# Optimization experiments

Measured on AMD Instinct MI355X. Metric: run time of the kernel, lower is better.

Reference implementation:

```python
import jax, jax.numpy as jnp
import numpy as np

MAX_WORDS = 50257
INPUT_SIZE = 1024
BATCH, SEQ = 8, 2048


def setup_inputs() -> dict:
    key = jax.random.key(0)
    kx, kw, kb = jax.random.split(key, 3)
    x = jax.random.randint(kx, (BATCH, SEQ), 0, MAX_WORDS, dtype=jnp.int64 if jax.config.jax_enable_x64 else jnp.int32)
    # nn.Linear(max_words, input_size): weight [input_size, max_words], bias [input_size]
    W = jax.random.normal(kw, (INPUT_SIZE, MAX_WORDS), dtype=jnp.float32) * 0.02
    b = jax.random.normal(kb, (INPUT_SIZE,), dtype=jnp.float32) * 0.02
    return {"x": x, "W": W, "b": b}


def reference(x, W, b):
    # one_hot(x, V).float() @ W.T + b  ==  gather rows of W.T at x, plus bias.
    # W.T has shape [max_words, input_size]; result [B, S, input_size].
    return jnp.take(W.T, x, axis=0) + b
```

## Files before the change

### kernel.cpp

```cpp
#include <hip/hip_runtime.h>


#define VOCAB 50257
#define DIM   1024
#define NBUCK ((VOCAB + 15) >> 4)
#define NXCD  8
#define TPB   64
#define JSL   128
#define NJS   (DIM / JSL)
#define TSTR  65


__global__ void hist_kernel(const int* __restrict__ x, int n, int* __restrict__ counts) {
    int i = blockIdx.x * blockDim.x + threadIdx.x;
    if (i < n) atomicAdd(&counts[x[i] >> 4], 1);
}

__global__ __launch_bounds__(256) void scan_kernel(const int* __restrict__ counts,
                                                   int* __restrict__ offs) {
    const int CHUNK = (NBUCK + 255) / 256;
    __shared__ int lds[256];
    const int tid = threadIdx.x;
    const int base = tid * CHUNK;
    int local[CHUNK];
    int s = 0;
#pragma unroll
    for (int k = 0; k < CHUNK; ++k) {
        int idx = base + k;
        int c = (idx < NBUCK) ? counts[idx] : 0;
        local[k] = s;
        s += c;
    }
    lds[tid] = s;
    __syncthreads();
    if (tid == 0) {
        int run = 0;
        for (int i = 0; i < 256; ++i) { int c = lds[i]; lds[i] = run; run += c; }
    }
    __syncthreads();
    const int boff = lds[tid];
#pragma unroll
    for (int k = 0; k < CHUNK; ++k) {
        int idx = base + k;
        if (idx < NBUCK) offs[idx] = boff + local[k];
    }
}

__global__ void scatter_kernel(const int* __restrict__ x, int n,
                               int* __restrict__ offs, int* __restrict__ order) {
    int i = blockIdx.x * blockDim.x + threadIdx.x;
    if (i < n) {
        int v = x[i];
        int pos = atomicAdd(&offs[v >> 4], 1);
        order[pos] = (v << 16) | i;
    }
}

__global__ __launch_bounds__(256) void lane_sorted_gather(
    const float* __restrict__ W,
    const float* __restrict__ bias,
    const int* __restrict__ order,
    float* __restrict__ out,
    int n, int q, int r)
{
    extern __shared__ float lds[];
    float* tile = lds;
    int* tTok = (int*)(lds + TPB * TSTR);

    const int bid = blockIdx.x;
    const int xcd = bid & (NXCD - 1);
    const int idx = bid >> 3;
    const int chunk_base = (xcd < r) ? xcd * (q + 1) : r * (q + 1) + (xcd - r) * q;
    const int L = chunk_base + idx;
    const int g  = L >> 3;
    const int js = L & 7;

    const int tid = threadIdx.x;
    const int wave = tid >> 6;
    const int lane = tid & 63;

    const int t0 = g * TPB;
    const int cnt = min(TPB, n - t0);

    const unsigned pk = (unsigned)order[t0 + (lane < cnt ? lane : 0)];
    const int vl = (int)(pk >> 16);
    if (wave == 0) tTok[lane] = (int)(pk & 0xFFFFu);

    const int jb0 = js * JSL;
    const float* __restrict__ Wv = W + vl;
    const int jw = jb0 + wave * 16;
    const int tok = tid >> 2;
    const int qq = tid & 3;

    float a0[8], b0[8];
#pragma unroll
    for (int i = 0; i < 8; ++i) a0[i] = Wv[(size_t)(jw + i) * VOCAB];
#pragma unroll
    for (int i = 0; i < 8; ++i) b0[i] = Wv[(size_t)(jw + 8 + i) * VOCAB];
    __builtin_amdgcn_sched_barrier(0);
#pragma unroll
    for (int i = 0; i < 8; ++i) tile[lane * TSTR + wave * 16 + i] = a0[i];
#pragma unroll
    for (int i = 0; i < 8; ++i) tile[lane * TSTR + wave * 16 + 8 + i] = b0[i];

    float a1[8], b1[8];
#pragma unroll
    for (int i = 0; i < 8; ++i) a1[i] = Wv[(size_t)(jw + 64 + i) * VOCAB];
#pragma unroll
    for (int i = 0; i < 8; ++i) b1[i] = Wv[(size_t)(jw + 72 + i) * VOCAB];
    __builtin_amdgcn_sched_barrier(0);

    __syncthreads();

    const int t_out = (tok < cnt) ? tTok[tok] : -1;
    if (t_out >= 0) {
        float* __restrict__ dst = out + (size_t)t_out * DIM + jb0;
#pragma unroll
        for (int k = 0; k < 4; ++k) {
            const int jloc = k * 16 + qq * 4;
            float4 w4 = *reinterpret_cast<const float4*>(&tile[tok * TSTR + jloc]);
            const float4 b4 = *reinterpret_cast<const float4*>(&bias[jb0 + jloc]);
            w4.x += b4.x; w4.y += b4.y; w4.z += b4.z; w4.w += b4.w;
            *reinterpret_cast<float4*>(dst + jloc) = w4;
        }
    }
    __syncthreads();

#pragma unroll
    for (int i = 0; i < 8; ++i) tile[lane * TSTR + wave * 16 + i] = a1[i];
#pragma unroll
    for (int i = 0; i < 8; ++i) tile[lane * TSTR + wave * 16 + 8 + i] = b1[i];
    __syncthreads();

    if (t_out >= 0) {
        float* __restrict__ dst = out + (size_t)t_out * DIM + jb0 + 64;
#pragma unroll
        for (int k = 0; k < 4; ++k) {
            const int jloc = k * 16 + qq * 4;
            float4 w4 = *reinterpret_cast<const float4*>(&tile[tok * TSTR + jloc]);
            const float4 b4 = *reinterpret_cast<const float4*>(&bias[jb0 + 64 + jloc]);
            w4.x += b4.x; w4.y += b4.y; w4.z += b4.z; w4.w += b4.w;
            *reinterpret_cast<float4*>(dst + jloc) = w4;
        }
    }
}

__global__ __launch_bounds__(256) void gather_direct_kernel(
    const int* __restrict__ x,
    const float* __restrict__ W,
    const float* __restrict__ bias,
    float* __restrict__ out)
{
    const int t = blockIdx.x;
    const int v = x[t];
    const int j0 = threadIdx.x * 4;
    float4 rr;
    rr.x = W[(size_t)(j0 + 0) * VOCAB + v];
    rr.y = W[(size_t)(j0 + 1) * VOCAB + v];
    rr.z = W[(size_t)(j0 + 2) * VOCAB + v];
    rr.w = W[(size_t)(j0 + 3) * VOCAB + v];
    const float4 bb = *reinterpret_cast<const float4*>(bias + j0);
    rr.x += bb.x; rr.y += bb.y; rr.z += bb.z; rr.w += bb.w;
    *reinterpret_cast<float4*>(out + (size_t)t * DIM + j0) = rr;
}

extern "C" void kernel_launch(void* const* d_in, const int* in_sizes, int n_in,
                              void* d_out, int out_size, void* d_ws, size_t ws_size,
                              hipStream_t stream) {
    const int*   x    = (const int*)d_in[0];
    const float* W    = (const float*)d_in[1];
    const float* bias = (const float*)d_in[2];
    float*       out  = (float*)d_out;

    const int n = in_sizes[0];

    const size_t need = (size_t)(2 * NBUCK + n) * sizeof(int);
    if (ws_size < need || n > 65536) {
        gather_direct_kernel<<<n, 256, 0, stream>>>(x, W, bias, out);
        return;
    }

    int* counts = (int*)d_ws;
    int* offs   = counts + NBUCK;
    int* order  = offs + NBUCK;

    const int tb = 256;
    hipMemsetAsync(counts, 0, NBUCK * sizeof(int), stream);
    hist_kernel<<<(n + tb - 1) / tb, tb, 0, stream>>>(x, n, counts);
    scan_kernel<<<1, tb, 0, stream>>>(counts, offs);
    scatter_kernel<<<(n + tb - 1) / tb, tb, 0, stream>>>(x, n, offs, order);

    const int ngroups = (n + TPB - 1) / TPB;
    const int nblk = ngroups * NJS;
    const int q = nblk / NXCD, r = nblk % NXCD;
    const size_t lds_bytes = (TPB * TSTR) * sizeof(float) + TPB * sizeof(int);
    lane_sorted_gather<<<nblk, 256, lds_bytes, stream>>>(W, bias, order, out, n, q, r);
}
```

Baseline: 65.70 us.

## Fuse memset, histogram and scan into one single-block LDS kernel

Replaces the memset, global-atomic histogram kernel and scan kernel with one 1024-thread block that builds the bucket histogram in LDS and computes the exclusive scan with wave shuffles. This removes two launches, a memset, and the global atomics plus the round trip through the counts array. In exchange, the histogram of all 16K tokens now runs on a single CU, which serializes that work.

Result: faster. 60.00 us (-8.7%).

```diff
diff --git a/kernel.cpp b/kernel.cpp
--- a/kernel.cpp
+++ b/kernel.cpp
@@ -10,39 +10,51 @@
 #define NJS   (DIM / JSL)
 #define TSTR  65
 
-
-__global__ void hist_kernel(const int* __restrict__ x, int n, int* __restrict__ counts) {
-    int i = blockIdx.x * blockDim.x + threadIdx.x;
-    if (i < n) atomicAdd(&counts[x[i] >> 4], 1);
-}
-
-__global__ __launch_bounds__(256) void scan_kernel(const int* __restrict__ counts,
-                                                   int* __restrict__ offs) {
-    const int CHUNK = (NBUCK + 255) / 256;
-    __shared__ int lds[256];
+__global__ __launch_bounds__(1024) void sort_prep_kernel(
+    const int* __restrict__ x, int n, int* __restrict__ offs)
+{
+    __shared__ int counts[NBUCK];
+    __shared__ int wtot[16];
+    __shared__ int wbase[16];
+
     const int tid = threadIdx.x;
-    const int base = tid * CHUNK;
-    int local[CHUNK];
-    int s = 0;
-#pragma unroll
-    for (int k = 0; k < CHUNK; ++k) {
-        int idx = base + k;
-        int c = (idx < NBUCK) ? counts[idx] : 0;
-        local[k] = s;
-        s += c;
-    }
-    lds[tid] = s;
-    __syncthreads();
-    if (tid == 0) {
-        int run = 0;
-        for (int i = 0; i < 256; ++i) { int c = lds[i]; lds[i] = run; run += c; }
-    }
-    __syncthreads();
-    const int boff = lds[tid];
-#pragma unroll
-    for (int k = 0; k < CHUNK; ++k) {
-        int idx = base + k;
-        if (idx < NBUCK) offs[idx] = boff + local[k];
+
+    for (int i = tid; i < NBUCK; i += 1024) counts[i] = 0;
+    __syncthreads();
+
+    for (int i = tid; i < n; i += 1024)
+        atomicAdd(&counts[((unsigned)x[i]) >> 4], 1);
+    __syncthreads();
+
+    int c[4];
+    const int b0 = tid * 4;
+#pragma unroll
+    for (int k = 0; k < 4; ++k)
+        c[k] = (b0 + k < NBUCK) ? counts[b0 + k] : 0;
+    const int partial = c[0] + c[1] + c[2] + c[3];
+
+    const int wave = tid >> 6, lane = tid & 63;
+    int s = partial;
+    for (int d = 1; d < 64; d <<= 1) {
+        int y = __shfl_up(s, d);
+        if (lane >= d) s += y;
+    }
+    if (lane == 63) wtot[wave] = s;
+    __syncthreads();
+    if (tid < 16) {
+        int v = wtot[tid];
+        int e = 0;
+        for (int w = 0; w < 16; ++w) { if (w == tid) break; e += wtot[w]; }
+        (void)v;
+        wbase[tid] = e;
+    }
+    __syncthreads();
+
+    int excl = wbase[wave] + s - partial;
+#pragma unroll
+    for (int k = 0; k < 4; ++k) {
+        if (b0 + k < NBUCK) offs[b0 + k] = excl;
+        excl += c[k];
     }
 }
 
@@ -174,20 +186,17 @@
 
     const int n = in_sizes[0];
 
-    const size_t need = (size_t)(2 * NBUCK + n) * sizeof(int);
+    const size_t need = (size_t)(NBUCK + n) * sizeof(int);
     if (ws_size < need || n > 65536) {
         gather_direct_kernel<<<n, 256, 0, stream>>>(x, W, bias, out);
         return;
     }
 
-    int* counts = (int*)d_ws;
-    int* offs   = counts + NBUCK;
+    int* offs   = (int*)d_ws;
     int* order  = offs + NBUCK;
 
+    sort_prep_kernel<<<1, 1024, 0, stream>>>(x, n, offs);
     const int tb = 256;
-    hipMemsetAsync(counts, 0, NBUCK * sizeof(int), stream);
-    hist_kernel<<<(n + tb - 1) / tb, tb, 0, stream>>>(x, n, counts);
-    scan_kernel<<<1, tb, 0, stream>>>(counts, offs);
     scatter_kernel<<<(n + tb - 1) / tb, tb, 0, stream>>>(x, n, offs, order);
 
     const int ngroups = (n + TPB - 1) / TPB;
```
